# Kernel tuning notes

Hardware: AMD Instinct MI355X
Metric: run time of the kernel (lower is better)

## Reference

```python
import jax, jax.numpy as jnp
import numpy as np

KS = 15       # erosion kernel size (ones kernel -> flat erosion = local min)
R = 60        # guided filter box-blur size
EPS = 1e-4


def _box_blur(x, r):
    # kornia box_blur: same-size mean filter, reflect padding; even kernel pads
    # (r-1)//2 before and r-1-(r-1)//2 after, per kornia _compute_padding.
    pb = (r - 1) // 2
    pa = r - 1 - pb
    xp = jnp.pad(x, ((0, 0), (0, 0), (pb, pa), (pb, pa)), mode='reflect')
    one = jnp.asarray(0.0, x.dtype)
    s = jax.lax.reduce_window(xp, one, jax.lax.add, (1, 1, r, 1), (1, 1, 1, 1), 'VALID')
    s = jax.lax.reduce_window(s, one, jax.lax.add, (1, 1, 1, r), (1, 1, 1, 1), 'VALID')
    return s / jnp.asarray(r * r, x.dtype)


def _erosion(x, k):
    # kornia flat erosion with ones kernel, geodesic border: local min over kxk
    p = k // 2
    init = jnp.asarray(jnp.inf, x.dtype)
    pad = [(0, 0), (0, 0), (p, p), (p, p)]
    e = jax.lax.reduce_window(x, init, jax.lax.min, (1, 1, k, 1), (1, 1, 1, 1), [(0, 0), (0, 0), (p, p), (0, 0)])
    e = jax.lax.reduce_window(e, init, jax.lax.min, (1, 1, 1, k), (1, 1, 1, 1), [(0, 0), (0, 0), (0, 0), (p, p)])
    return e


def setup_inputs() -> dict:
    key = jax.random.key(0)
    I = jax.random.uniform(key, (8, 3, 1080, 1920), dtype=jnp.float32)
    return {"I": I}


def reference(I) -> jnp.ndarray:
    # dark channel: per-pixel min over the 3 channels  [B,1,H,W]
    dark = jnp.min(I, axis=1, keepdims=True)
    # guided_filter_plus(dark)
    d_im = _erosion(dark, KS)
    mean_I = _box_blur(d_im, R)
    mean_p = _box_blur(dark, R)
    mean_Ip = _box_blur(d_im * dark, R)
    cov_Ip = mean_Ip - mean_I * mean_p
    mean_II = _box_blur(d_im * d_im, R)
    var_I = mean_II - mean_I * mean_I
    a = cov_Ip / (var_I + EPS)
    b = mean_p - a * mean_I
    mean_a = _box_blur(a, R)
    mean_b = _box_blur(b, R)
    q = mean_a * d_im + mean_b
    return q
```

## Files before the change

### kernel.cpp

```cpp
#include <hip/hip_runtime.h>
#include <hip/hip_fp16.h>

#define HH 1080
#define WW 1920
#define NB 8
#define HWP (HH*WW)
#define NPXs ((size_t)NB*HWP)
#define NC4 (WW/4)

#define PADI(e) ((e) + ((e) >> 5))

__device__ __forceinline__ int reflH(int y){ int r = y < 0 ? -y : y; return r >= HH ? 2*HH-2-r : r; }
__device__ __forceinline__ int reflW(int x){ int r = x < 0 ? -x : x; return r >= WW ? 2*WW-2-r : r; }

__device__ __forceinline__ unsigned pkmin(unsigned a, unsigned b){
    unsigned r; asm("v_pk_min_f16 %0, %1, %2" : "=v"(r) : "v"(a), "v"(b)); return r;
}
#define INF2 0x7C007C00u

__global__ __launch_bounds__(256) void k_dark_eh(const float* __restrict__ I,
                                                 __half* __restrict__ dark, __half* __restrict__ eh){
    __shared__ float ds[2048];
    int bid = blockIdx.x;
    int y = bid % HH;
    int b = bid / HH;
    const float* row0 = I + (size_t)b*3*HWP + (size_t)y*WW;
    size_t rb = (size_t)b*HWP + (size_t)y*WW;
    int tid = threadIdx.x;
    if (tid < 240){
        int x0 = tid*8;
        float4 c00 = *(const float4*)(row0 + x0);
        float4 c01 = *(const float4*)(row0 + x0 + 4);
        float4 c10 = *(const float4*)(row0 + HWP + x0);
        float4 c11 = *(const float4*)(row0 + HWP + x0 + 4);
        float4 c20 = *(const float4*)(row0 + 2*HWP + x0);
        float4 c21 = *(const float4*)(row0 + 2*HWP + x0 + 4);
        float m[8];
        m[0]=fminf(fminf(c00.x,c10.x),c20.x); m[1]=fminf(fminf(c00.y,c10.y),c20.y);
        m[2]=fminf(fminf(c00.z,c10.z),c20.z); m[3]=fminf(fminf(c00.w,c10.w),c20.w);
        m[4]=fminf(fminf(c01.x,c11.x),c21.x); m[5]=fminf(fminf(c01.y,c11.y),c21.y);
        m[6]=fminf(fminf(c01.z,c11.z),c21.z); m[7]=fminf(fminf(c01.w,c11.w),c21.w);
        __half2 hd[4];
        #pragma unroll
        for (int l=0;l<4;++l) hd[l] = __floats2half2_rn(m[2*l], m[2*l+1]);
        *(uint4*)(dark + rb + x0) = *(uint4*)hd;
        #pragma unroll
        for (int i=0;i<8;++i) ds[PADI(x0+7+i)] = m[i];
    } else if (tid == 240){
        for (int i=0;i<7;++i) ds[PADI(i)] = 1e30f;
    } else if (tid == 241){
        for (int i=0;i<7;++i) ds[PADI(1927+i)] = 1e30f;
    }
    __syncthreads();
    if (tid >= 240) return;
    int x0 = tid*8;
    float s[22];
    #pragma unroll
    for (int i=0;i<22;++i) s[i] = ds[PADI(x0+i)];
    float t1[21], t2[19], t4[15];
    #pragma unroll
    for (int i=0;i<21;++i) t1[i] = fminf(s[i], s[i+1]);
    #pragma unroll
    for (int i=0;i<19;++i) t2[i] = fminf(t1[i], t1[i+2]);
    #pragma unroll
    for (int i=0;i<15;++i) t4[i] = fminf(t2[i], t2[i+4]);
    __half2 ho[4];
    #pragma unroll
    for (int l=0;l<4;++l){
        float o0 = fminf(t4[2*l],   t4[2*l+7]);
        float o1 = fminf(t4[2*l+1], t4[2*l+8]);
        ho[l] = __floats2half2_rn(o0, o1);
    }
    *(uint4*)(eh + rb + x0) = *(uint4*)ho;
}

__global__ __launch_bounds__(256) void k_erosv(const __half* __restrict__ eh, __half* __restrict__ dim){
    int t = blockIdx.x*256 + threadIdx.x;
    int c4 = t % NC4;
    int r  = t / NC4;
    int b  = r & 7;
    int y0 = (r >> 3) * 15;
    const __half* sp = eh  + (size_t)b*HWP + (size_t)c4*4;
    __half*       dp = dim + (size_t)b*HWP + (size_t)c4*4;
    uint2 s[15];
    #pragma unroll
    for (int j=0;j<15;++j){
        int y = y0 - 7 + j;
        if ((unsigned)y < HH) s[j] = *(const uint2*)(sp + (size_t)y*WW);
        else { s[j].x = INF2; s[j].y = INF2; }
    }
    #pragma unroll
    for (int j=13;j>=0;--j){
        s[j].x = pkmin(s[j].x, s[j+1].x); s[j].y = pkmin(s[j].y, s[j+1].y);
    }
    *(uint2*)(dp + (size_t)y0*WW) = s[0];
    uint2 P; P.x = INF2; P.y = INF2;
    #pragma unroll
    for (int j=1;j<15;++j){
        int y = y0 + 7 + j;
        uint2 nv;
        if ((unsigned)y < HH) nv = *(const uint2*)(sp + (size_t)y*WW);
        else { nv.x = INF2; nv.y = INF2; }
        P.x = pkmin(P.x, nv.x); P.y = pkmin(P.y, nv.y);
        uint2 o;
        o.x = pkmin(s[j].x, P.x); o.y = pkmin(s[j].y, P.y);
        *(uint2*)(dp + (size_t)(y0+j)*WW) = o;
    }
}

#define BT 18
__global__ __launch_bounds__(256) void k_blurv4(const __half* __restrict__ dimp, const __half* __restrict__ darkp,
                                                __half* __restrict__ m0, __half* __restrict__ m1,
                                                __half* __restrict__ m2, __half* __restrict__ m3){
    int t = blockIdx.x*256 + threadIdx.x;
    int c4 = t % NC4;
    int r  = t / NC4;
    int b  = r & 7;
    int y0 = (r >> 3) * BT;
    size_t base = (size_t)b*HWP + (size_t)c4*4;
    const __half* pd = dimp + base;
    const __half* pk = darkp + base;
    float sI[4], sP[4], sIP[4], sII[4];
    #pragma unroll
    for (int i=0;i<4;++i){ sI[i]=0.f; sP[i]=0.f; sIP[i]=0.f; sII[i]=0.f; }
    auto accA = [&](int yy){
        int yr = reflH(yy);
        uint2 vd = *(const uint2*)(pd + (size_t)yr*WW);
        uint2 vk = *(const uint2*)(pk + (size_t)yr*WW);
        const __half2* hd = (const __half2*)&vd;
        const __half2* hk = (const __half2*)&vk;
        #pragma unroll
        for (int l=0;l<2;++l){
            float2 fd = __half22float2(hd[l]);
            float2 fk = __half22float2(hk[l]);
            sI[2*l]+=fd.x; sI[2*l+1]+=fd.y;
            sP[2*l]+=fk.x; sP[2*l+1]+=fk.y;
            sIP[2*l]+=fd.x*fk.x; sIP[2*l+1]+=fd.y*fk.y;
            sII[2*l]+=fd.x*fd.x; sII[2*l+1]+=fd.y*fd.y;
        }
    };
    auto accS = [&](int yy){
        int yr = reflH(yy);
        uint2 vd = *(const uint2*)(pd + (size_t)yr*WW);
        uint2 vk = *(const uint2*)(pk + (size_t)yr*WW);
        const __half2* hd = (const __half2*)&vd;
        const __half2* hk = (const __half2*)&vk;
        #pragma unroll
        for (int l=0;l<2;++l){
            float2 fd = __half22float2(hd[l]);
            float2 fk = __half22float2(hk[l]);
            sI[2*l]-=fd.x; sI[2*l+1]-=fd.y;
            sP[2*l]-=fk.x; sP[2*l+1]-=fk.y;
            sIP[2*l]-=fd.x*fk.x; sIP[2*l+1]-=fd.y*fk.y;
            sII[2*l]-=fd.x*fd.x; sII[2*l+1]-=fd.y*fd.y;
        }
    };
    const float inv = 1.0f/60.0f;
    for (int k=-29;k<=30;++k) accA(y0+k);
    auto emit = [&](int y){
        size_t off = base + (size_t)y*WW;
        __half2 h[2];
        h[0]=__floats2half2_rn(sI[0]*inv,sI[1]*inv);  h[1]=__floats2half2_rn(sI[2]*inv,sI[3]*inv);
        *(uint2*)(m0+off) = *(uint2*)h;
        h[0]=__floats2half2_rn(sP[0]*inv,sP[1]*inv);  h[1]=__floats2half2_rn(sP[2]*inv,sP[3]*inv);
        *(uint2*)(m1+off) = *(uint2*)h;
        h[0]=__floats2half2_rn(sIP[0]*inv,sIP[1]*inv); h[1]=__floats2half2_rn(sIP[2]*inv,sIP[3]*inv);
        *(uint2*)(m2+off) = *(uint2*)h;
        h[0]=__floats2half2_rn(sII[0]*inv,sII[1]*inv); h[1]=__floats2half2_rn(sII[2]*inv,sII[3]*inv);
        *(uint2*)(m3+off) = *(uint2*)h;
    };
    emit(y0);
    for (int y=y0+1; y<y0+BT; ++y){
        accA(y+30);
        accS(y-30);
        emit(y);
    }
}

__global__ __launch_bounds__(256) void k_hab(const __half* __restrict__ m0, const __half* __restrict__ m1,
                                             const __half* __restrict__ m2, const __half* __restrict__ m3,
                                             __half* __restrict__ aH, __half* __restrict__ bH){
    __shared__ float4 PA[4][256];
    __shared__ float4 PB[4][256];
    __shared__ float4 QA[2][264];
    __shared__ float4 QB[2][264];
    __shared__ float wt[4][4];
    __shared__ float wt2[2][4];

    int bid = blockIdx.x;
    int y = bid % HH;
    int b = bid / HH;
    size_t rb = (size_t)b*HWP + (size_t)y*WW;
    int tid = threadIdx.x;
    int lane = tid & 63;
    int wv = tid >> 6;

    const __half* mp0 = m0 + rb; const __half* mp1 = m1 + rb;
    const __half* mp2 = m2 + rb; const __half* mp3 = m3 + rb;

    float xv[4][8];
    int u = tid;
    if (u >= 4 && u <= 243){
        int x0 = 8*(u-4);
        const __half* mp[4] = {mp0, mp1, mp2, mp3};
        #pragma unroll
        for (int p=0;p<4;++p){
            uint4 hv = *(const uint4*)(mp[p] + x0);
            const __half2* h2 = (const __half2*)&hv;
            #pragma unroll
            for (int l=0;l<4;++l){
                float2 f = __half22float2(h2[l]);
                xv[p][2*l] = f.x; xv[p][2*l+1] = f.y;
            }
        }
    } else {
        #pragma unroll
        for (int i=0;i<8;++i){
            int s = 8*u + i;
            if (s >= 3 && s <= 1981){
                int j = s - 3;
                int x = j - 29;
                if (x < 0) x = -x;
                else if (x > 1919) x = 3838 - x;
                xv[0][i] = __half2float(mp0[x]);
                xv[1][i] = __half2float(mp1[x]);
                xv[2][i] = __half2float(mp2[x]);
                xv[3][i] = __half2float(mp3[x]);
            } else {
                xv[0][i]=0.f; xv[1][i]=0.f; xv[2][i]=0.f; xv[3][i]=0.f;
            }
        }
    }

    float ebase[4];
    #pragma unroll
    for (int p=0;p<4;++p){
        #pragma unroll
        for (int i=1;i<8;++i) xv[p][i] += xv[p][i-1];
        float v = xv[p][7];
        #pragma unroll
        for (int d=1; d<64; d<<=1){
            float tmp = __shfl_up(v, d);
            if (lane >= d) v += tmp;
        }
        ebase[p] = v - xv[p][7];
        if (lane == 63) wt[p][wv] = v;
    }
    __syncthreads();
    #pragma unroll
    for (int p=0;p<4;++p){
        float bb = ebase[p];
        if (wv > 0) bb += wt[p][0];
        if (wv > 1) bb += wt[p][1];
        if (wv > 2) bb += wt[p][2];
        #pragma unroll
        for (int i=0;i<8;++i) xv[p][i] += bb;
        if (u > 0) *((float2*)&PB[p][u-1] + 1) = make_float2(xv[p][0], xv[p][1]);
        PA[p][u] = make_float4(xv[p][2], xv[p][3], xv[p][4], xv[p][5]);
        *((float2*)&PB[p][u]) = make_float2(xv[p][6], xv[p][7]);
    }
    __syncthreads();

    float Aa[8], Bb[8];
    int t = tid;
    if (t < 240){
        const float inv = 1.0f/60.0f;
        float mm[4][8];
        #pragma unroll
        for (int p=0;p<4;++p){
            float4 loa = PA[p][t];
            float4 lob = PB[p][t];
            float4 hib = PB[p][t+7];
            float4 hia = PA[p][t+8];
            mm[p][0]=(hib.x-loa.x)*inv; mm[p][1]=(hib.y-loa.y)*inv;
            mm[p][2]=(hib.z-loa.z)*inv; mm[p][3]=(hib.w-loa.w)*inv;
            mm[p][4]=(hia.x-lob.x)*inv; mm[p][5]=(hia.y-lob.y)*inv;
            mm[p][6]=(hia.z-lob.z)*inv; mm[p][7]=(hia.w-lob.w)*inv;
        }
        #pragma unroll
        for (int i=0;i<8;++i){
            float mI=mm[0][i], mP=mm[1][i], mIp=mm[2][i], mII=mm[3][i];
            float cov = mIp - mI*mP;
            float var = mII - mI*mI;
            float a = cov / (var + 1e-4f);
            Aa[i] = a;
            Bb[i] = mP - a*mI;
        }
    } else {
        #pragma unroll
        for (int i=0;i<8;++i){ Aa[i]=0.f; Bb[i]=0.f; }
    }

    float eA, eB;
    {
        #pragma unroll
        for (int i=1;i<8;++i) Aa[i] += Aa[i-1];
        float v = Aa[7];
        #pragma unroll
        for (int d=1; d<64; d<<=1){
            float tmp = __shfl_up(v, d);
            if (lane >= d) v += tmp;
        }
        eA = v - Aa[7];
        if (lane==63) wt2[0][wv] = v;
    }
    {
        #pragma unroll
        for (int i=1;i<8;++i) Bb[i] += Bb[i-1];
        float v = Bb[7];
        #pragma unroll
        for (int d=1; d<64; d<<=1){
            float tmp = __shfl_up(v, d);
            if (lane >= d) v += tmp;
        }
        eB = v - Bb[7];
        if (lane==63) wt2[1][wv] = v;
    }
    __syncthreads();
    {
        float bb = eA;
        if (wv>0) bb += wt2[0][0];
        if (wv>1) bb += wt2[0][1];
        if (wv>2) bb += wt2[0][2];
        #pragma unroll
        for (int i=0;i<8;++i) Aa[i] += bb;
        bb = eB;
        if (wv>0) bb += wt2[1][0];
        if (wv>1) bb += wt2[1][1];
        if (wv>2) bb += wt2[1][2];
        #pragma unroll
        for (int i=0;i<8;++i) Bb[i] += bb;
    }
    *((float2*)&QB[0][t+3] + 1) = make_float2(Aa[0], Aa[1]);
    QA[0][t+4] = make_float4(Aa[2], Aa[3], Aa[4], Aa[5]);
    *((float2*)&QB[0][t+4]) = make_float2(Aa[6], Aa[7]);
    *((float2*)&QB[1][t+3] + 1) = make_float2(Bb[0], Bb[1]);
    QA[1][t+4] = make_float4(Bb[2], Bb[3], Bb[4], Bb[5]);
    *((float2*)&QB[1][t+4]) = make_float2(Bb[6], Bb[7]);
    if (tid >= 248){
        int k = tid - 248;
        float4 z4 = make_float4(0.f,0.f,0.f,0.f);
        if (k < 4){ QA[0][k] = z4; QA[1][k] = z4; }
        else if (k < 7){ QB[0][k-4] = z4; QB[1][k-4] = z4; }
        else { *((float2*)&QB[0][3]) = make_float2(0.f,0.f);
               *((float2*)&QB[1][3]) = make_float2(0.f,0.f); }
    }
    __syncthreads();
    if (t >= 240) return;

    int x0 = 8*t;
    float4 lA0 = QA[0][t];   float4 lA1 = QB[0][t];
    float4 hA0 = QB[0][t+7]; float4 hA1 = QA[0][t+8];
    float4 lB0 = QA[1][t];   float4 lB1 = QB[1][t];
    float4 hB0 = QB[1][t+7]; float4 hB1 = QA[1][t+8];
    float sA[8], sB[8];
    sA[0]=hA0.x-lA0.x; sA[1]=hA0.y-lA0.y; sA[2]=hA0.z-lA0.z; sA[3]=hA0.w-lA0.w;
    sA[4]=hA1.x-lA1.x; sA[5]=hA1.y-lA1.y; sA[6]=hA1.z-lA1.z; sA[7]=hA1.w-lA1.w;
    sB[0]=hB0.x-lB0.x; sB[1]=hB0.y-lB0.y; sB[2]=hB0.z-lB0.z; sB[3]=hB0.w-lB0.w;
    sB[4]=hB1.x-lB1.x; sB[5]=hB1.y-lB1.y; sB[6]=hB1.z-lB1.z; sB[7]=hB1.w-lB1.w;

    auto prRead = [&](int pl, int v)->float{
        int z = v + 30;
        int c = z >> 2;
        float4 f = (c & 1) ? QB[pl][c>>1] : QA[pl][c>>1];
        int w = z & 3;
        return (w==0)?f.x:((w==1)?f.y:((w==2)?f.z:f.w));
    };
    if (x0 < 29){
        #pragma unroll
        for (int i=0;i<8;++i){
            int x = x0 + i;
            if (x < 29){
                sA[i] += prRead(0, 29-x) - prRead(0, 0);
                sB[i] += prRead(1, 29-x) - prRead(1, 0);
            }
        }
    }
    if (x0 + 7 > 1889){
        #pragma unroll
        for (int i=0;i<8;++i){
            int x = x0 + i;
            if (x > 1889){
                sA[i] += prRead(0, 1918) - prRead(0, 3807-x);
                sB[i] += prRead(1, 1918) - prRead(1, 3807-x);
            }
        }
    }
    const float inv = 1.0f/60.0f;
    __half2 ha[4], hb[4];
    #pragma unroll
    for (int l=0;l<4;++l){
        ha[l] = __floats2half2_rn(sA[2*l]*inv, sA[2*l+1]*inv);
        hb[l] = __floats2half2_rn(sB[2*l]*inv, sB[2*l+1]*inv);
    }
    *(uint4*)(aH + rb + x0) = *(uint4*)ha;
    *(uint4*)(bH + rb + x0) = *(uint4*)hb;
}

__global__ __launch_bounds__(256) void k_final(const __half* __restrict__ aHp, const __half* __restrict__ bHp,
                                               const __half* __restrict__ dimp, float* __restrict__ q){
    int t = blockIdx.x*256 + threadIdx.x;
    int c4 = t % NC4;
    int r  = t / NC4;
    int b  = r & 7;
    int y0 = (r >> 3) * BT;
    size_t base = (size_t)b*HWP + (size_t)c4*4;
    const __half* pa = aHp + base;
    const __half* pb = bHp + base;
    const __half* pd = dimp + base;
    float* pq = q + base;
    float sa[4], sb[4];
    #pragma unroll
    for (int i=0;i<4;++i){ sa[i]=0.f; sb[i]=0.f; }
    auto accA = [&](int yy){
        int yr = reflH(yy);
        uint2 va = *(const uint2*)(pa + (size_t)yr*WW);
        uint2 vb = *(const uint2*)(pb + (size_t)yr*WW);
        const __half2* hA = (const __half2*)&va;
        const __half2* hB = (const __half2*)&vb;
        #pragma unroll
        for (int l=0;l<2;++l){
            float2 fa = __half22float2(hA[l]);
            float2 fb = __half22float2(hB[l]);
            sa[2*l]+=fa.x; sa[2*l+1]+=fa.y;
            sb[2*l]+=fb.x; sb[2*l+1]+=fb.y;
        }
    };
    auto accS = [&](int yy){
        int yr = reflH(yy);
        uint2 va = *(const uint2*)(pa + (size_t)yr*WW);
        uint2 vb = *(const uint2*)(pb + (size_t)yr*WW);
        const __half2* hA = (const __half2*)&va;
        const __half2* hB = (const __half2*)&vb;
        #pragma unroll
        for (int l=0;l<2;++l){
            float2 fa = __half22float2(hA[l]);
            float2 fb = __half22float2(hB[l]);
            sa[2*l]-=fa.x; sa[2*l+1]-=fa.y;
            sb[2*l]-=fb.x; sb[2*l+1]-=fb.y;
        }
    };
    const float inv = 1.0f/60.0f;
    for (int k=-29;k<=30;++k) accA(y0+k);
    auto emit = [&](int y){
        uint2 vd = *(const uint2*)(pd + (size_t)y*WW);
        const __half2* hd = (const __half2*)&vd;
        float2 f0 = __half22float2(hd[0]);
        float2 f1 = __half22float2(hd[1]);
        float4 o;
        o.x = (sa[0]*inv)*f0.x + sb[0]*inv;
        o.y = (sa[1]*inv)*f0.y + sb[1]*inv;
        o.z = (sa[2]*inv)*f1.x + sb[2]*inv;
        o.w = (sa[3]*inv)*f1.y + sb[3]*inv;
        *(float4*)(pq + (size_t)y*WW) = o;
    };
    emit(y0);
    for (int y=y0+1; y<y0+BT; ++y){
        accA(y+30);
        accS(y-30);
        emit(y);
    }
}

extern "C" void kernel_launch(void* const* d_in, const int* in_sizes, int n_in,
                              void* d_out, int out_size, void* d_ws, size_t ws_size,
                              hipStream_t stream){
    const float* I = (const float*)d_in[0];
    float* qout = (float*)d_out;
    __half* ws = (__half*)d_ws;

    __half* p_dark = ws;
    __half* p_eh   = ws + NPXs;
    __half* p_dim  = ws + 2*NPXs;
    __half* p_m0   = ws + 3*NPXs;
    __half* p_m1   = ws + 4*NPXs;
    __half* p_m2   = ws + 5*NPXs;
    __half* p_m3   = ws + 6*NPXs;
    __half* p_aH   = p_dark;
    __half* p_bH   = p_eh;

    k_dark_eh<<<NB*HH, 256, 0, stream>>>(I, p_dark, p_eh);
    k_erosv  <<<1080,  256, 0, stream>>>(p_eh, p_dim);
    k_blurv4 <<<900,   256, 0, stream>>>(p_dim, p_dark, p_m0, p_m1, p_m2, p_m3);
    k_hab    <<<NB*HH, 256, 0, stream>>>(p_m0, p_m1, p_m2, p_m3, p_aH, p_bH);
    k_final  <<<900,   256, 0, stream>>>(p_aH, p_bH, p_dim, qout);
}
```

Measured before the change: 285.9 us.

## Fuse vertical box-blur of four moments into the horizontal a/b kernel

Merges the vertical running-sum blur kernel with the per-row horizontal blur and a/b computation. Each block now handles an 18-row strip of full width and keeps the vertical sums in registers. The four intermediate fp16 moment planes are therefore never written to or read from global memory. The cost is fewer blocks (480), extra syncthreads per row inside a serial loop, and scattered loads for the reflected border columns.

```diff
diff --git a/kernel.cpp b/kernel.cpp
--- a/kernel.cpp
+++ b/kernel.cpp
@@ -11,7 +11,6 @@
 #define PADI(e) ((e) + ((e) >> 5))
 
 __device__ __forceinline__ int reflH(int y){ int r = y < 0 ? -y : y; return r >= HH ? 2*HH-2-r : r; }
-__device__ __forceinline__ int reflW(int x){ int r = x < 0 ? -x : x; return r >= WW ? 2*WW-2-r : r; }
 
 __device__ __forceinline__ unsigned pkmin(unsigned a, unsigned b){
     unsigned r; asm("v_pk_min_f16 %0, %1, %2" : "=v"(r) : "v"(a), "v"(b)); return r;
@@ -108,78 +107,9 @@
     }
 }
 
-#define BT 18
-__global__ __launch_bounds__(256) void k_blurv4(const __half* __restrict__ dimp, const __half* __restrict__ darkp,
-                                                __half* __restrict__ m0, __half* __restrict__ m1,
-                                                __half* __restrict__ m2, __half* __restrict__ m3){
-    int t = blockIdx.x*256 + threadIdx.x;
-    int c4 = t % NC4;
-    int r  = t / NC4;
-    int b  = r & 7;
-    int y0 = (r >> 3) * BT;
-    size_t base = (size_t)b*HWP + (size_t)c4*4;
-    const __half* pd = dimp + base;
-    const __half* pk = darkp + base;
-    float sI[4], sP[4], sIP[4], sII[4];
-    #pragma unroll
-    for (int i=0;i<4;++i){ sI[i]=0.f; sP[i]=0.f; sIP[i]=0.f; sII[i]=0.f; }
-    auto accA = [&](int yy){
-        int yr = reflH(yy);
-        uint2 vd = *(const uint2*)(pd + (size_t)yr*WW);
-        uint2 vk = *(const uint2*)(pk + (size_t)yr*WW);
-        const __half2* hd = (const __half2*)&vd;
-        const __half2* hk = (const __half2*)&vk;
-        #pragma unroll
-        for (int l=0;l<2;++l){
-            float2 fd = __half22float2(hd[l]);
-            float2 fk = __half22float2(hk[l]);
-            sI[2*l]+=fd.x; sI[2*l+1]+=fd.y;
-            sP[2*l]+=fk.x; sP[2*l+1]+=fk.y;
-            sIP[2*l]+=fd.x*fk.x; sIP[2*l+1]+=fd.y*fk.y;
-            sII[2*l]+=fd.x*fd.x; sII[2*l+1]+=fd.y*fd.y;
-        }
-    };
-    auto accS = [&](int yy){
-        int yr = reflH(yy);
-        uint2 vd = *(const uint2*)(pd + (size_t)yr*WW);
-        uint2 vk = *(const uint2*)(pk + (size_t)yr*WW);
-        const __half2* hd = (const __half2*)&vd;
-        const __half2* hk = (const __half2*)&vk;
-        #pragma unroll
-        for (int l=0;l<2;++l){
-            float2 fd = __half22float2(hd[l]);
-            float2 fk = __half22float2(hk[l]);
-            sI[2*l]-=fd.x; sI[2*l+1]-=fd.y;
-            sP[2*l]-=fk.x; sP[2*l+1]-=fk.y;
-            sIP[2*l]-=fd.x*fk.x; sIP[2*l+1]-=fd.y*fk.y;
-            sII[2*l]-=fd.x*fd.x; sII[2*l+1]-=fd.y*fd.y;
-        }
-    };
-    const float inv = 1.0f/60.0f;
-    for (int k=-29;k<=30;++k) accA(y0+k);
-    auto emit = [&](int y){
-        size_t off = base + (size_t)y*WW;
-        __half2 h[2];
-        h[0]=__floats2half2_rn(sI[0]*inv,sI[1]*inv);  h[1]=__floats2half2_rn(sI[2]*inv,sI[3]*inv);
-        *(uint2*)(m0+off) = *(uint2*)h;
-        h[0]=__floats2half2_rn(sP[0]*inv,sP[1]*inv);  h[1]=__floats2half2_rn(sP[2]*inv,sP[3]*inv);
-        *(uint2*)(m1+off) = *(uint2*)h;
-        h[0]=__floats2half2_rn(sIP[0]*inv,sIP[1]*inv); h[1]=__floats2half2_rn(sIP[2]*inv,sIP[3]*inv);
-        *(uint2*)(m2+off) = *(uint2*)h;
-        h[0]=__floats2half2_rn(sII[0]*inv,sII[1]*inv); h[1]=__floats2half2_rn(sII[2]*inv,sII[3]*inv);
-        *(uint2*)(m3+off) = *(uint2*)h;
-    };
-    emit(y0);
-    for (int y=y0+1; y<y0+BT; ++y){
-        accA(y+30);
-        accS(y-30);
-        emit(y);
-    }
-}
-
-__global__ __launch_bounds__(256) void k_hab(const __half* __restrict__ m0, const __half* __restrict__ m1,
-                                             const __half* __restrict__ m2, const __half* __restrict__ m3,
-                                             __half* __restrict__ aH, __half* __restrict__ bH){
+#define VT 18
+__global__ __launch_bounds__(256) void k_vh(const __half* __restrict__ dimp, const __half* __restrict__ darkp,
+                                            __half* __restrict__ aH, __half* __restrict__ bH){
     __shared__ float4 PA[4][256];
     __shared__ float4 PB[4][256];
     __shared__ float4 QA[2][264];
@@ -188,215 +118,243 @@
     __shared__ float wt2[2][4];
 
     int bid = blockIdx.x;
-    int y = bid % HH;
-    int b = bid / HH;
-    size_t rb = (size_t)b*HWP + (size_t)y*WW;
+    int yt = bid % (HH/VT);
+    int b  = bid / (HH/VT);
+    int y0 = yt * VT;
+    size_t pbase = (size_t)b*HWP;
+    const __half* pd = dimp  + pbase;
+    const __half* pk = darkp + pbase;
     int tid = threadIdx.x;
-    int lane = tid & 63;
-    int wv = tid >> 6;
-
-    const __half* mp0 = m0 + rb; const __half* mp1 = m1 + rb;
-    const __half* mp2 = m2 + rb; const __half* mp3 = m3 + rb;
-
-    float xv[4][8];
-    int u = tid;
-    if (u >= 4 && u <= 243){
-        int x0 = 8*(u-4);
-        const __half* mp[4] = {mp0, mp1, mp2, mp3};
-        #pragma unroll
-        for (int p=0;p<4;++p){
-            uint4 hv = *(const uint4*)(mp[p] + x0);
-            const __half2* h2 = (const __half2*)&hv;
+    int lane = tid & 63, wv = tid >> 6;
+
+    bool interior = (tid >= 4 && tid <= 243);
+    int x0i = 8*(tid-4);
+    int cols[8]; bool valid[8]; bool anyv = false;
+    #pragma unroll
+    for (int i=0;i<8;++i){
+        int s = 8*tid + i;
+        if (s >= 3 && s <= 1981){
+            int j = s - 3;
+            cols[i] = (j < 29) ? (29 - j) : ((j <= 1948) ? (j - 29) : (3867 - j));
+            valid[i] = true; anyv = true;
+        } else { cols[i] = 0; valid[i] = false; }
+    }
+
+    float sI[8], sP[8], sIP[8], sII[8];
+    #pragma unroll
+    for (int i=0;i<8;++i){ sI[i]=0.f; sP[i]=0.f; sIP[i]=0.f; sII[i]=0.f; }
+
+    auto addrow = [&](int yy, float sg){
+        int yr = reflH(yy);
+        size_t ro = (size_t)yr*WW;
+        if (interior){
+            uint4 vd = *(const uint4*)(pd + ro + x0i);
+            uint4 vk = *(const uint4*)(pk + ro + x0i);
+            const __half2* hd = (const __half2*)&vd;
+            const __half2* hk = (const __half2*)&vk;
             #pragma unroll
             for (int l=0;l<4;++l){
-                float2 f = __half22float2(h2[l]);
-                xv[p][2*l] = f.x; xv[p][2*l+1] = f.y;
-            }
-        }
-    } else {
-        #pragma unroll
-        for (int i=0;i<8;++i){
-            int s = 8*u + i;
-            if (s >= 3 && s <= 1981){
-                int j = s - 3;
-                int x = j - 29;
-                if (x < 0) x = -x;
-                else if (x > 1919) x = 3838 - x;
-                xv[0][i] = __half2float(mp0[x]);
-                xv[1][i] = __half2float(mp1[x]);
-                xv[2][i] = __half2float(mp2[x]);
-                xv[3][i] = __half2float(mp3[x]);
-            } else {
-                xv[0][i]=0.f; xv[1][i]=0.f; xv[2][i]=0.f; xv[3][i]=0.f;
-            }
-        }
-    }
-
-    float ebase[4];
-    #pragma unroll
-    for (int p=0;p<4;++p){
-        #pragma unroll
-        for (int i=1;i<8;++i) xv[p][i] += xv[p][i-1];
-        float v = xv[p][7];
-        #pragma unroll
-        for (int d=1; d<64; d<<=1){
-            float tmp = __shfl_up(v, d);
-            if (lane >= d) v += tmp;
-        }
-        ebase[p] = v - xv[p][7];
-        if (lane == 63) wt[p][wv] = v;
-    }
-    __syncthreads();
-    #pragma unroll
-    for (int p=0;p<4;++p){
-        float bb = ebase[p];
-        if (wv > 0) bb += wt[p][0];
-        if (wv > 1) bb += wt[p][1];
-        if (wv > 2) bb += wt[p][2];
-        #pragma unroll
-        for (int i=0;i<8;++i) xv[p][i] += bb;
-        if (u > 0) *((float2*)&PB[p][u-1] + 1) = make_float2(xv[p][0], xv[p][1]);
-        PA[p][u] = make_float4(xv[p][2], xv[p][3], xv[p][4], xv[p][5]);
-        *((float2*)&PB[p][u]) = make_float2(xv[p][6], xv[p][7]);
-    }
-    __syncthreads();
-
-    float Aa[8], Bb[8];
-    int t = tid;
-    if (t < 240){
-        const float inv = 1.0f/60.0f;
-        float mm[4][8];
-        #pragma unroll
-        for (int p=0;p<4;++p){
-            float4 loa = PA[p][t];
-            float4 lob = PB[p][t];
-            float4 hib = PB[p][t+7];
-            float4 hia = PA[p][t+8];
-            mm[p][0]=(hib.x-loa.x)*inv; mm[p][1]=(hib.y-loa.y)*inv;
-            mm[p][2]=(hib.z-loa.z)*inv; mm[p][3]=(hib.w-loa.w)*inv;
-            mm[p][4]=(hia.x-lob.x)*inv; mm[p][5]=(hia.y-lob.y)*inv;
-            mm[p][6]=(hia.z-lob.z)*inv; mm[p][7]=(hia.w-lob.w)*inv;
-        }
-        #pragma unroll
-        for (int i=0;i<8;++i){
-            float mI=mm[0][i], mP=mm[1][i], mIp=mm[2][i], mII=mm[3][i];
-            float cov = mIp - mI*mP;
-            float var = mII - mI*mI;
-            float a = cov / (var + 1e-4f);
-            Aa[i] = a;
-            Bb[i] = mP - a*mI;
-        }
-    } else {
-        #pragma unroll
-        for (int i=0;i<8;++i){ Aa[i]=0.f; Bb[i]=0.f; }
-    }
-
-    float eA, eB;
-    {
-        #pragma unroll
-        for (int i=1;i<8;++i) Aa[i] += Aa[i-1];
-        float v = Aa[7];
-        #pragma unroll
-        for (int d=1; d<64; d<<=1){
-            float tmp = __shfl_up(v, d);
-            if (lane >= d) v += tmp;
-        }
-        eA = v - Aa[7];
-        if (lane==63) wt2[0][wv] = v;
-    }
-    {
-        #pragma unroll
-        for (int i=1;i<8;++i) Bb[i] += Bb[i-1];
-        float v = Bb[7];
-        #pragma unroll
-        for (int d=1; d<64; d<<=1){
-            float tmp = __shfl_up(v, d);
-            if (lane >= d) v += tmp;
-        }
-        eB = v - Bb[7];
-        if (lane==63) wt2[1][wv] = v;
-    }
-    __syncthreads();
-    {
-        float bb = eA;
-        if (wv>0) bb += wt2[0][0];
-        if (wv>1) bb += wt2[0][1];
-        if (wv>2) bb += wt2[0][2];
-        #pragma unroll
-        for (int i=0;i<8;++i) Aa[i] += bb;
-        bb = eB;
-        if (wv>0) bb += wt2[1][0];
-        if (wv>1) bb += wt2[1][1];
-        if (wv>2) bb += wt2[1][2];
-        #pragma unroll
-        for (int i=0;i<8;++i) Bb[i] += bb;
-    }
-    *((float2*)&QB[0][t+3] + 1) = make_float2(Aa[0], Aa[1]);
-    QA[0][t+4] = make_float4(Aa[2], Aa[3], Aa[4], Aa[5]);
-    *((float2*)&QB[0][t+4]) = make_float2(Aa[6], Aa[7]);
-    *((float2*)&QB[1][t+3] + 1) = make_float2(Bb[0], Bb[1]);
-    QA[1][t+4] = make_float4(Bb[2], Bb[3], Bb[4], Bb[5]);
-    *((float2*)&QB[1][t+4]) = make_float2(Bb[6], Bb[7]);
+                float2 fd = __half22float2(hd[l]);
+                float2 fk = __half22float2(hk[l]);
+                sI[2*l]   += sg*fd.x;        sI[2*l+1]  += sg*fd.y;
+                sP[2*l]   += sg*fk.x;        sP[2*l+1]  += sg*fk.y;
+                sIP[2*l]  += sg*(fd.x*fk.x); sIP[2*l+1] += sg*(fd.y*fk.y);
+                sII[2*l]  += sg*(fd.x*fd.x); sII[2*l+1] += sg*(fd.y*fd.y);
+            }
+        } else if (anyv){
+            #pragma unroll
+            for (int i=0;i<8;++i){
+                if (valid[i]){
+                    float d = __half2float(pd[ro + cols[i]]);
+                    float k = __half2float(pk[ro + cols[i]]);
+                    sI[i] += sg*d; sP[i] += sg*k; sIP[i] += sg*(d*k); sII[i] += sg*(d*d);
+                }
+            }
+        }
+    };
+
+    for (int k=-29;k<=30;++k) addrow(y0+k, 1.0f);
+
     if (tid >= 248){
-        int k = tid - 248;
+        int k2 = tid - 248;
         float4 z4 = make_float4(0.f,0.f,0.f,0.f);
-        if (k < 4){ QA[0][k] = z4; QA[1][k] = z4; }
-        else if (k < 7){ QB[0][k-4] = z4; QB[1][k-4] = z4; }
+        if (k2 < 4){ QA[0][k2] = z4; QA[1][k2] = z4; }
+        else if (k2 < 7){ QB[0][k2-4] = z4; QB[1][k2-4] = z4; }
         else { *((float2*)&QB[0][3]) = make_float2(0.f,0.f);
                *((float2*)&QB[1][3]) = make_float2(0.f,0.f); }
     }
-    __syncthreads();
-    if (t >= 240) return;
-
-    int x0 = 8*t;
-    float4 lA0 = QA[0][t];   float4 lA1 = QB[0][t];
-    float4 hA0 = QB[0][t+7]; float4 hA1 = QA[0][t+8];
-    float4 lB0 = QA[1][t];   float4 lB1 = QB[1][t];
-    float4 hB0 = QB[1][t+7]; float4 hB1 = QA[1][t+8];
-    float sA[8], sB[8];
-    sA[0]=hA0.x-lA0.x; sA[1]=hA0.y-lA0.y; sA[2]=hA0.z-lA0.z; sA[3]=hA0.w-lA0.w;
-    sA[4]=hA1.x-lA1.x; sA[5]=hA1.y-lA1.y; sA[6]=hA1.z-lA1.z; sA[7]=hA1.w-lA1.w;
-    sB[0]=hB0.x-lB0.x; sB[1]=hB0.y-lB0.y; sB[2]=hB0.z-lB0.z; sB[3]=hB0.w-lB0.w;
-    sB[4]=hB1.x-lB1.x; sB[5]=hB1.y-lB1.y; sB[6]=hB1.z-lB1.z; sB[7]=hB1.w-lB1.w;
-
-    auto prRead = [&](int pl, int v)->float{
-        int z = v + 30;
-        int c = z >> 2;
-        float4 f = (c & 1) ? QB[pl][c>>1] : QA[pl][c>>1];
-        int w = z & 3;
-        return (w==0)?f.x:((w==1)?f.y:((w==2)?f.z:f.w));
-    };
-    if (x0 < 29){
+
+    const float inv = 1.0f/60.0f;
+    for (int y=y0; y<y0+VT; ++y){
+        if (y > y0){ addrow(y+30, 1.0f); addrow(y-30, -1.0f); }
+
+        float xv[4][8];
         #pragma unroll
         for (int i=0;i<8;++i){
-            int x = x0 + i;
-            if (x < 29){
-                sA[i] += prRead(0, 29-x) - prRead(0, 0);
-                sB[i] += prRead(1, 29-x) - prRead(1, 0);
-            }
-        }
-    }
-    if (x0 + 7 > 1889){
-        #pragma unroll
-        for (int i=0;i<8;++i){
-            int x = x0 + i;
-            if (x > 1889){
-                sA[i] += prRead(0, 1918) - prRead(0, 3807-x);
-                sB[i] += prRead(1, 1918) - prRead(1, 3807-x);
-            }
-        }
-    }
-    const float inv = 1.0f/60.0f;
-    __half2 ha[4], hb[4];
-    #pragma unroll
-    for (int l=0;l<4;++l){
-        ha[l] = __floats2half2_rn(sA[2*l]*inv, sA[2*l+1]*inv);
-        hb[l] = __floats2half2_rn(sB[2*l]*inv, sB[2*l+1]*inv);
-    }
-    *(uint4*)(aH + rb + x0) = *(uint4*)ha;
-    *(uint4*)(bH + rb + x0) = *(uint4*)hb;
-}
-
+            xv[0][i] = sI[i]*inv;
+            xv[1][i] = sP[i]*inv;
+            xv[2][i] = sIP[i]*inv;
+            xv[3][i] = sII[i]*inv;
+        }
+
+        float ebase[4];
+        #pragma unroll
+        for (int p=0;p<4;++p){
+            #pragma unroll
+            for (int i=1;i<8;++i) xv[p][i] += xv[p][i-1];
+            float v = xv[p][7];
+            #pragma unroll
+            for (int d=1; d<64; d<<=1){
+                float tmp = __shfl_up(v, d);
+                if (lane >= d) v += tmp;
+            }
+            ebase[p] = v - xv[p][7];
+            if (lane == 63) wt[p][wv] = v;
+        }
+        __syncthreads();
+        #pragma unroll
+        for (int p=0;p<4;++p){
+            float bb = ebase[p];
+            if (wv > 0) bb += wt[p][0];
+            if (wv > 1) bb += wt[p][1];
+            if (wv > 2) bb += wt[p][2];
+            #pragma unroll
+            for (int i=0;i<8;++i) xv[p][i] += bb;
+            if (tid > 0) *((float2*)&PB[p][tid-1] + 1) = make_float2(xv[p][0], xv[p][1]);
+            PA[p][tid] = make_float4(xv[p][2], xv[p][3], xv[p][4], xv[p][5]);
+            *((float2*)&PB[p][tid]) = make_float2(xv[p][6], xv[p][7]);
+        }
+        __syncthreads();
+
+        float Aa[8], Bb[8];
+        if (tid < 240){
+            float mm[4][8];
+            #pragma unroll
+            for (int p=0;p<4;++p){
+                float4 loa = PA[p][tid];
+                float4 lob = PB[p][tid];
+                float4 hib = PB[p][tid+7];
+                float4 hia = PA[p][tid+8];
+                mm[p][0]=(hib.x-loa.x)*inv; mm[p][1]=(hib.y-loa.y)*inv;
+                mm[p][2]=(hib.z-loa.z)*inv; mm[p][3]=(hib.w-loa.w)*inv;
+                mm[p][4]=(hia.x-lob.x)*inv; mm[p][5]=(hia.y-lob.y)*inv;
+                mm[p][6]=(hia.z-lob.z)*inv; mm[p][7]=(hia.w-lob.w)*inv;
+            }
+            #pragma unroll
+            for (int i=0;i<8;++i){
+                float mI=mm[0][i], mP=mm[1][i], mIp=mm[2][i], mII=mm[3][i];
+                float cov = mIp - mI*mP;
+                float var = mII - mI*mI;
+                float a = cov / (var + 1e-4f);
+                Aa[i] = a;
+                Bb[i] = mP - a*mI;
+            }
+        } else {
+            #pragma unroll
+            for (int i=0;i<8;++i){ Aa[i]=0.f; Bb[i]=0.f; }
+        }
+
+        float eA, eB;
+        {
+            #pragma unroll
+            for (int i=1;i<8;++i) Aa[i] += Aa[i-1];
+            float v = Aa[7];
+            #pragma unroll
+            for (int d=1; d<64; d<<=1){
+                float tmp = __shfl_up(v, d);
+                if (lane >= d) v += tmp;
+            }
+            eA = v - Aa[7];
+            if (lane==63) wt2[0][wv] = v;
+        }
+        {
+            #pragma unroll
+            for (int i=1;i<8;++i) Bb[i] += Bb[i-1];
+            float v = Bb[7];
+            #pragma unroll
+            for (int d=1; d<64; d<<=1){
+                float tmp = __shfl_up(v, d);
+                if (lane >= d) v += tmp;
+            }
+            eB = v - Bb[7];
+            if (lane==63) wt2[1][wv] = v;
+        }
+        __syncthreads();
+        {
+            float bb = eA;
+            if (wv>0) bb += wt2[0][0];
+            if (wv>1) bb += wt2[0][1];
+            if (wv>2) bb += wt2[0][2];
+            #pragma unroll
+            for (int i=0;i<8;++i) Aa[i] += bb;
+            bb = eB;
+            if (wv>0) bb += wt2[1][0];
+            if (wv>1) bb += wt2[1][1];
+            if (wv>2) bb += wt2[1][2];
+            #pragma unroll
+            for (int i=0;i<8;++i) Bb[i] += bb;
+        }
+        *((float2*)&QB[0][tid+3] + 1) = make_float2(Aa[0], Aa[1]);
+        QA[0][tid+4] = make_float4(Aa[2], Aa[3], Aa[4], Aa[5]);
+        *((float2*)&QB[0][tid+4]) = make_float2(Aa[6], Aa[7]);
+        *((float2*)&QB[1][tid+3] + 1) = make_float2(Bb[0], Bb[1]);
+        QA[1][tid+4] = make_float4(Bb[2], Bb[3], Bb[4], Bb[5]);
+        *((float2*)&QB[1][tid+4]) = make_float2(Bb[6], Bb[7]);
+        __syncthreads();
+
+        if (tid < 240){
+            int x0 = 8*tid;
+            float4 lA0 = QA[0][tid];   float4 lA1 = QB[0][tid];
+            float4 hA0 = QB[0][tid+7]; float4 hA1 = QA[0][tid+8];
+            float4 lB0 = QA[1][tid];   float4 lB1 = QB[1][tid];
+            float4 hB0 = QB[1][tid+7]; float4 hB1 = QA[1][tid+8];
+            float sA[8], sB[8];
+            sA[0]=hA0.x-lA0.x; sA[1]=hA0.y-lA0.y; sA[2]=hA0.z-lA0.z; sA[3]=hA0.w-lA0.w;
+            sA[4]=hA1.x-lA1.x; sA[5]=hA1.y-lA1.y; sA[6]=hA1.z-lA1.z; sA[7]=hA1.w-lA1.w;
+            sB[0]=hB0.x-lB0.x; sB[1]=hB0.y-lB0.y; sB[2]=hB0.z-lB0.z; sB[3]=hB0.w-lB0.w;
+            sB[4]=hB1.x-lB1.x; sB[5]=hB1.y-lB1.y; sB[6]=hB1.z-lB1.z; sB[7]=hB1.w-lB1.w;
+
+            auto prRead = [&](int pl, int v)->float{
+                int z = v + 30;
+                int c = z >> 2;
+                float4 f = (c & 1) ? QB[pl][c>>1] : QA[pl][c>>1];
+                int w = z & 3;
+                return (w==0)?f.x:((w==1)?f.y:((w==2)?f.z:f.w));
+            };
+            if (x0 < 29){
+                #pragma unroll
+                for (int i=0;i<8;++i){
+                    int x = x0 + i;
+                    if (x < 29){
+                        sA[i] += prRead(0, 29-x) - prRead(0, 0);
+                        sB[i] += prRead(1, 29-x) - prRead(1, 0);
+                    }
+                }
+            }
+            if (x0 + 7 > 1889){
+                #pragma unroll
+                for (int i=0;i<8;++i){
+                    int x = x0 + i;
+                    if (x > 1889){
+                        sA[i] += prRead(0, 1918) - prRead(0, 3807-x);
+                        sB[i] += prRead(1, 1918) - prRead(1, 3807-x);
+                    }
+                }
+            }
+            __half2 ha[4], hb[4];
+            #pragma unroll
+            for (int l=0;l<4;++l){
+                ha[l] = __floats2half2_rn(sA[2*l]*inv, sA[2*l+1]*inv);
+                hb[l] = __floats2half2_rn(sB[2*l]*inv, sB[2*l+1]*inv);
+            }
+            size_t ro = pbase + (size_t)y*WW + x0;
+            *(uint4*)(aH + ro) = *(uint4*)ha;
+            *(uint4*)(bH + ro) = *(uint4*)hb;
+        }
+    }
+}
+
+#define BT 18
 __global__ __launch_bounds__(256) void k_final(const __half* __restrict__ aHp, const __half* __restrict__ bHp,
                                                const __half* __restrict__ dimp, float* __restrict__ q){
     int t = blockIdx.x*256 + threadIdx.x;
@@ -472,16 +430,11 @@
     __half* p_dark = ws;
     __half* p_eh   = ws + NPXs;
     __half* p_dim  = ws + 2*NPXs;
-    __half* p_m0   = ws + 3*NPXs;
-    __half* p_m1   = ws + 4*NPXs;
-    __half* p_m2   = ws + 5*NPXs;
-    __half* p_m3   = ws + 6*NPXs;
-    __half* p_aH   = p_dark;
-    __half* p_bH   = p_eh;
-
-    k_dark_eh<<<NB*HH, 256, 0, stream>>>(I, p_dark, p_eh);
-    k_erosv  <<<1080,  256, 0, stream>>>(p_eh, p_dim);
-    k_blurv4 <<<900,   256, 0, stream>>>(p_dim, p_dark, p_m0, p_m1, p_m2, p_m3);
-    k_hab    <<<NB*HH, 256, 0, stream>>>(p_m0, p_m1, p_m2, p_m3, p_aH, p_bH);
-    k_final  <<<900,   256, 0, stream>>>(p_aH, p_bH, p_dim, qout);
-}
+    __half* p_aH   = ws + 3*NPXs;
+    __half* p_bH   = ws + 4*NPXs;
+
+    k_dark_eh<<<NB*HH,         256, 0, stream>>>(I, p_dark, p_eh);
+    k_erosv  <<<1080,          256, 0, stream>>>(p_eh, p_dim);
+    k_vh     <<<NB*(HH/VT),    256, 0, stream>>>(p_dim, p_dark, p_aH, p_bH);
+    k_final  <<<900,           256, 0, stream>>>(p_aH, p_bH, p_dim, qout);
+}
```

Result: slower. 367.7 us (+28.6%).
